# Optimization experiments

Hardware: AMD Instinct MI355X
Metric: run time of the kernel (lower is better)

Reference implementation:

```python
import jax, jax.numpy as jnp
import numpy as np

D = 512
H = 8
DV = D // H  # 64
NEG_INF = -1e30


def setup_inputs() -> dict:
    key = jax.random.key(0)
    ks = jax.random.split(key, 10)
    B, S = 4, 2048
    x = jax.random.normal(ks[0], (B, D, S), dtype=jnp.float32)
    mask = jnp.ones((B, S), dtype=jnp.float32)
    s = 1.0 / np.sqrt(D)
    sv = 1.0 / np.sqrt(D)
    # per-head Linear(d -> dv) weights stacked: [H, dv, d] (torch Linear layout W @ x)
    Wq = jax.random.uniform(ks[1], (H, DV, D), jnp.float32, -s, s)
    bq = jax.random.uniform(ks[2], (H, DV), jnp.float32, -s, s)
    Wk = jax.random.uniform(ks[3], (H, DV, D), jnp.float32, -s, s)
    bk = jax.random.uniform(ks[4], (H, DV), jnp.float32, -s, s)
    Wv = jax.random.uniform(ks[5], (H, DV, D), jnp.float32, -s, s)
    bv = jax.random.uniform(ks[6], (H, DV), jnp.float32, -s, s)
    W0 = jax.random.uniform(ks[7], (D, D), jnp.float32, -sv, sv)
    b0 = jax.random.uniform(ks[8], (D,), jnp.float32, -sv, sv)
    return {"x": x, "mask": mask, "Wq": Wq, "bq": bq, "Wk": Wk, "bk": bk,
            "Wv": Wv, "bv": bv, "W0": W0, "b0": b0}


def reference(x, mask, Wq, bq, Wk, bk, Wv, bv, W0, b0):
    # x: [B, d, S] -> xt: [B, S, d]
    xt = jnp.transpose(x, (0, 2, 1))
    # fused per-head projections: [B, H, S, dv]
    q = jnp.einsum('bsd,hed->bhse', xt, Wq) + bq[None, :, None, :]
    k = jnp.einsum('bsd,hed->bhse', xt, Wk) + bk[None, :, None, :]
    v = jnp.einsum('bsd,hed->bhse', xt, Wv) + bv[None, :, None, :]
    dv = q.shape[-1]
    scores = jnp.einsum('bhse,bhte->bhst', q, k) * (1.0 / np.sqrt(dv))
    # mask_logits (QANet style): keep where mask==1, else -1e30; mask over key dim
    h_mask = mask[:, None, None, :]  # [B,1,1,S]
    scores = scores * h_mask + (1.0 - h_mask) * NEG_INF
    p = jax.nn.softmax(scores, axis=-1)
    # zero out fully-masked query rows via v_mask on query dim
    p = p * mask[:, None, :, None]
    out = jnp.einsum('bhst,bhte->bhse', p, v)  # [B,H,S,dv]
    # concat heads along feature dim -> [B, S, d]
    B, _, S, _ = out.shape
    heads = jnp.transpose(out, (0, 2, 1, 3)).reshape(B, S, -1)
    y = heads @ W0.T + b0  # output projection
    return jnp.transpose(y, (0, 2, 1))  # [B, d, S]
```

## Files before the change

### kernel.cpp

```cpp
#include <hip/hip_runtime.h>

#define B_  4
#define D_  512
#define H_  8
#define DV_ 64
#define S_  2048

typedef __bf16 bf16;
typedef bf16  bf16x8 __attribute__((ext_vector_type(8)));
typedef bf16  bf16x4 __attribute__((ext_vector_type(4)));
typedef float f32x4  __attribute__((ext_vector_type(4)));

#define MFMA(a, b, c) __builtin_amdgcn_mfma_f32_16x16x32_bf16((a), (b), (c), 0, 0, 0)

#define GLOAD_LDS(g, l)                                                     \
    __builtin_amdgcn_global_load_lds(                                       \
        (const __attribute__((address_space(1))) void*)(g),                 \
        (__attribute__((address_space(3))) void*)(l), 16, 0, 0)

#define WAIT_VMCNT(n)                                                       \
    __builtin_amdgcn_s_waitcnt(((n) & 15) | (((n) >> 4) << 14) | (7 << 4) | (15 << 8))

__global__ __launch_bounds__(256) void prep(
    const float* __restrict__ x, const float* __restrict__ Wq,
    const float* __restrict__ Wk, const float* __restrict__ Wv,
    const float* __restrict__ W0, bf16* __restrict__ xb, bf16* __restrict__ Wb) {
    const int bid = blockIdx.x;
    if (bid < 4096) {
        __shared__ float tile[32][33];
        const int sblk = bid % 64;
        const int dblk = (bid / 64) % 16;
        const int b    = bid / 1024;
        const int d0 = dblk * 32, s0 = sblk * 32;
        const int tx = threadIdx.x & 31;
        const int ty = threadIdx.x >> 5;
        const float* xp = x + (size_t)b * D_ * S_;
#pragma unroll
        for (int i = 0; i < 32; i += 8)
            tile[ty + i][tx] = xp[(size_t)(d0 + ty + i) * S_ + s0 + tx];
        __syncthreads();
        bf16* xbp = xb + ((size_t)b * S_ + s0) * D_ + d0;
#pragma unroll
        for (int i = 0; i < 32; i += 8)
            xbp[(size_t)(ty + i) * D_ + tx] = (bf16)tile[tx][ty + i];
    } else {
        const int f0 = ((bid - 4096) * 256 + threadIdx.x) * 16;
        const int src = f0 >> 18;
        const int off = f0 & 262143;
        const float* W = (src == 0) ? Wq : (src == 1) ? Wk : (src == 2) ? Wv : W0;
        float4 v0 = *(const float4*)&W[off];
        float4 v1 = *(const float4*)&W[off + 4];
        float4 v2 = *(const float4*)&W[off + 8];
        float4 v3 = *(const float4*)&W[off + 12];
        bf16x8 h0 = {(bf16)v0.x, (bf16)v0.y, (bf16)v0.z, (bf16)v0.w,
                     (bf16)v1.x, (bf16)v1.y, (bf16)v1.z, (bf16)v1.w};
        bf16x8 h1 = {(bf16)v2.x, (bf16)v2.y, (bf16)v2.z, (bf16)v2.w,
                     (bf16)v3.x, (bf16)v3.y, (bf16)v3.z, (bf16)v3.w};
        *(bf16x8*)&Wb[f0]     = h0;
        *(bf16x8*)&Wb[f0 + 8] = h1;
    }
}

__global__ __launch_bounds__(256) void gemm_qkv(
    const bf16* __restrict__ A, const bf16* __restrict__ Wb,
    const float* __restrict__ bq, const float* __restrict__ bk,
    const float* __restrict__ bv,
    bf16* __restrict__ Q, bf16* __restrict__ K, bf16* __restrict__ Vt) {
    __shared__ union {
        struct { bf16 A[8192]; bf16 B[8192]; } s;
        bf16 T[128][132];
    } sm;

    const int tid = threadIdx.x;
    const int w = tid >> 6, lane = tid & 63;
    const int m16 = lane & 15, quad = lane >> 4;
    const int wr = w & 1, wc = w >> 1;

    const int nblk = blockIdx.x % 12;
    const int mblk = blockIdx.x / 12;
    const int m0 = mblk * 128, n0 = nblk * 128;

    f32x4 acc[4][4];
#pragma unroll
    for (int i = 0; i < 4; ++i)
#pragma unroll
        for (int j = 0; j < 4; ++j) acc[i][j] = (f32x4){0.f, 0.f, 0.f, 0.f};

    for (int k0 = 0; k0 < D_; k0 += 64) {
        __syncthreads();
#pragma unroll
        for (int i = 0; i < 4; ++i) {
            const int c  = w * 4 + i;
            const int mt = c >> 1, kk = c & 1;
            const int row = mt * 16 + m16;
            const int col = k0 + kk * 32 + quad * 8;
            GLOAD_LDS(&A[(size_t)(m0 + row) * D_ + col],  &sm.s.A[(c * 64 + lane) * 8]);
            GLOAD_LDS(&Wb[(size_t)(n0 + row) * D_ + col], &sm.s.B[(c * 64 + lane) * 8]);
        }
        __syncthreads();
#pragma unroll
        for (int kk = 0; kk < 2; ++kk) {
            bf16x8 af[4], bfv[4];
#pragma unroll
            for (int t = 0; t < 4; ++t) {
                af[t]  = *(const bf16x8*)&sm.s.A[(((wr * 4 + t) * 2 + kk) * 64 + lane) * 8];
                bfv[t] = *(const bf16x8*)&sm.s.B[(((wc * 4 + t) * 2 + kk) * 64 + lane) * 8];
            }
#pragma unroll
            for (int mt = 0; mt < 4; ++mt)
#pragma unroll
                for (int nt = 0; nt < 4; ++nt)
                    acc[mt][nt] = MFMA(af[mt], bfv[nt], acc[mt][nt]);
        }
    }

    const int proj = n0 >> 9;
    const float* bias = (proj == 0) ? bq : (proj == 1) ? bk : bv;

    if (proj == 2) {
#pragma unroll
        for (int mt = 0; mt < 4; ++mt)
#pragma unroll
            for (int nt = 0; nt < 4; ++nt) {
                const int nr = (n0 + wc * 64 + nt * 16 + m16) & 511;
                const int h = nr >> 6, e = nr & 63;
                const float bia = bias[nr];
                const int srow = m0 + wr * 64 + mt * 16 + quad * 4;
                const int b = srow >> 11, s = srow & 2047;
                const int s2 = (s & ~31) | (quad * 8 + (mt & 1) * 4);
                bf16x4 hv;
#pragma unroll
                for (int r = 0; r < 4; ++r) hv[r] = (bf16)(acc[mt][nt][r] + bia);
                *(bf16x4*)&Vt[(((size_t)b * H_ + h) * DV_ + e) * S_ + s2] = hv;
            }
    } else {
        __syncthreads();
#pragma unroll
        for (int mt = 0; mt < 4; ++mt)
#pragma unroll
            for (int nt = 0; nt < 4; ++nt) {
                const int nloc = wc * 64 + nt * 16 + m16;
                const float bia = bias[(n0 + nloc) & 511];
#pragma unroll
                for (int r = 0; r < 4; ++r)
                    sm.T[wr * 64 + mt * 16 + quad * 4 + r][nloc] =
                        (bf16)(acc[mt][nt][r] + bia);
            }
        __syncthreads();
        const int rloc = tid >> 1, cb = (tid & 1) * 64;
        const int M = m0 + rloc, b = M >> 11, s = M & 2047;
        const int nrb = (n0 + cb) & 511;
        const int h = nrb >> 6;
        bf16* dst = ((proj == 0) ? Q : K) + (((size_t)b * H_ + h) * S_ + s) * DV_;
#pragma unroll
        for (int u = 0; u < 8; ++u)
            *(bf16x8*)&dst[u * 8] = *(const bf16x8*)&sm.T[rloc][cb + u * 8];
    }
}

__global__ __launch_bounds__(256, 2) void flash_attn(
    const bf16* __restrict__ Q, const bf16* __restrict__ K, const bf16* __restrict__ Vt,
    const float* __restrict__ mask, bf16* __restrict__ heads) {
    __shared__ union {
        struct {
            bf16 Kl[2][4][2048];
            bf16 Vl[2][4][2048];
            float Ms[2048];
        } s;
        struct { float O[64][65]; float L[64]; } red;
    } sm;

    const int bidx = blockIdx.x;
    const int qblk = bidx & 31;
    const int h    = (bidx >> 5) & 7;
    const int b    = bidx >> 8;
    const int q0   = qblk * 64;

    const int tid = threadIdx.x;
    const int w = tid >> 6, lane = tid & 63;
    const int m16 = lane & 15, quad = lane >> 4;

    const bf16* Qp = Q  + ((size_t)b * H_ + h) * S_ * DV_;
    const bf16* Kp = K  + ((size_t)b * H_ + h) * S_ * DV_;
    const bf16* Vp = Vt + ((size_t)b * H_ + h) * DV_ * S_;
    const float* mp = mask + (size_t)b * S_;

    const int krow = lane >> 3;
    const int kcol = ((lane & 7) ^ krow) * 8;
    const int vrow = lane >> 2;
    const int vcol = ((lane & 3) ^ (vrow & 3)) * 8;

    bf16x8 qf[4][2];
#pragma unroll
    for (int qt = 0; qt < 4; ++qt)
#pragma unroll
        for (int kk = 0; kk < 2; ++kk) {
            bf16x8 v = *(const bf16x8*)&Qp[(size_t)(q0 + qt * 16 + m16) * DV_ +
                                           kk * 32 + quad * 8];
#pragma unroll
            for (int i = 0; i < 8; ++i) v[i] = (bf16)((float)v[i] * 0.125f);
            qf[qt][kk] = v;
        }

    bf16x8 ones;
#pragma unroll
    for (int i = 0; i < 8; ++i) ones[i] = (bf16)1.0f;

    f32x4 o[4][4];
    f32x4 lacc[4];
#pragma unroll
    for (int mt = 0; mt < 4; ++mt)
#pragma unroll
        for (int qt = 0; qt < 4; ++qt) o[mt][qt] = (f32x4){0.f, 0.f, 0.f, 0.f};
#pragma unroll
    for (int qt = 0; qt < 4; ++qt) lacc[qt] = (f32x4){0.f, 0.f, 0.f, 0.f};

#pragma unroll
    for (int p = 0; p < 2; ++p)
        GLOAD_LDS(&mp[(p * 256 + tid) * 4], &sm.s.Ms[(p * 256 + tid) * 4]);
    {
        const int tw = w * 32;
#pragma unroll
        for (int p = 0; p < 4; ++p)
            GLOAD_LDS(&Kp[(size_t)(tw + p * 8 + krow) * DV_ + kcol],
                      &sm.s.Kl[0][w][(p * 64 + lane) * 8]);
#pragma unroll
        for (int p = 0; p < 4; ++p)
            GLOAD_LDS(&Vp[(size_t)(p * 16 + vrow) * S_ + tw + vcol],
                      &sm.s.Vl[0][w][(p * 64 + lane) * 8]);
    }
    __syncthreads();

    for (int i = 0; i < 16; ++i) {
        const int tw = i * 128 + w * 32;
        if (i < 15) {
            const int twn = tw + 128;
            const int nb = (i + 1) & 1;
#pragma unroll
            for (int p = 0; p < 4; ++p)
                GLOAD_LDS(&Kp[(size_t)(twn + p * 8 + krow) * DV_ + kcol],
                          &sm.s.Kl[nb][w][(p * 64 + lane) * 8]);
#pragma unroll
            for (int p = 0; p < 4; ++p)
                GLOAD_LDS(&Vp[(size_t)(p * 16 + vrow) * S_ + twn + vcol],
                          &sm.s.Vl[nb][w][(p * 64 + lane) * 8]);
            WAIT_VMCNT(8);
        } else {
            WAIT_VMCNT(0);
        }
        const int buf = i & 1;

        bf16x8 kf[2][2];
#pragma unroll
        for (int tt = 0; tt < 2; ++tt)
#pragma unroll
            for (int kk = 0; kk < 2; ++kk)
                kf[tt][kk] = *(const bf16x8*)&sm.s.Kl[buf][w][
                    ((tt * 16 + m16) * 8 + ((kk * 4 + quad) ^ (m16 & 7))) * 8];
        bf16x8 vf[4];
#pragma unroll
        for (int mt = 0; mt < 4; ++mt)
            vf[mt] = *(const bf16x8*)&sm.s.Vl[buf][w][
                ((mt * 16 + m16) * 4 + (quad ^ (m16 & 3))) * 8];
        const f32x4 mq0 = *(const f32x4*)&sm.s.Ms[tw + quad * 4];
        const f32x4 mq1 = *(const f32x4*)&sm.s.Ms[tw + 16 + quad * 4];

        f32x4 sc[2][4];
#pragma unroll
        for (int tt = 0; tt < 2; ++tt)
#pragma unroll
            for (int qt = 0; qt < 4; ++qt) sc[tt][qt] = (f32x4){0.f, 0.f, 0.f, 0.f};
#pragma unroll
        for (int kk = 0; kk < 2; ++kk)
#pragma unroll
            for (int tt = 0; tt < 2; ++tt)
#pragma unroll
                for (int qt = 0; qt < 4; ++qt)
                    sc[tt][qt] = MFMA(kf[tt][kk], qf[qt][kk], sc[tt][qt]);

        f32x4 ng0, ng1;
#pragma unroll
        for (int r = 0; r < 4; ++r) {
            ng0[r] = (1.0f - mq0[r]) * -1e30f;
            ng1[r] = (1.0f - mq1[r]) * -1e30f;
        }
        bf16x8 pf[4];
#pragma unroll
        for (int qt = 0; qt < 4; ++qt)
#pragma unroll
            for (int r = 0; r < 4; ++r) {
                pf[qt][r]     = (bf16)__expf(sc[0][qt][r] * mq0[r] + ng0[r]);
                pf[qt][4 + r] = (bf16)__expf(sc[1][qt][r] * mq1[r] + ng1[r]);
            }

#pragma unroll
        for (int mt = 0; mt < 4; ++mt)
#pragma unroll
            for (int qt = 0; qt < 4; ++qt) o[mt][qt] = MFMA(vf[mt], pf[qt], o[mt][qt]);
#pragma unroll
        for (int qt = 0; qt < 4; ++qt) lacc[qt] = MFMA(ones, pf[qt], lacc[qt]);
    }

    __syncthreads();
#pragma unroll
    for (int ww = 0; ww < 4; ++ww) {
        if (w == ww) {
#pragma unroll
            for (int mt = 0; mt < 4; ++mt)
#pragma unroll
                for (int qt = 0; qt < 4; ++qt)
#pragma unroll
                    for (int r = 0; r < 4; ++r) {
                        float* slot = &sm.red.O[mt * 16 + quad * 4 + r][qt * 16 + m16];
                        *slot = (ww == 0) ? o[mt][qt][r] : (*slot + o[mt][qt][r]);
                    }
            if (quad == 0)
#pragma unroll
                for (int qt = 0; qt < 4; ++qt) {
                    float* ls = &sm.red.L[qt * 16 + m16];
                    *ls = (ww == 0) ? lacc[qt][0] : (*ls + lacc[qt][0]);
                }
        }
        __syncthreads();
    }

    const int ql = tid >> 2, ec = (tid & 3) * 16;
    const float l  = sm.red.L[ql];
    const float qm = mp[q0 + ql];
    const float inv = qm / l;
    bf16x8 hv[2];
#pragma unroll
    for (int c = 0; c < 2; ++c)
#pragma unroll
        for (int i = 0; i < 8; ++i)
            hv[c][i] = (bf16)(sm.red.O[ec + c * 8 + i][ql] * inv);
    bf16* dst = &heads[((size_t)b * S_ + q0 + ql) * D_ + h * DV_ + ec];
    *(bf16x8*)(dst)     = hv[0];
    *(bf16x8*)(dst + 8) = hv[1];
}

__global__ __launch_bounds__(256) void gemm_out(
    const bf16* __restrict__ A, const bf16* __restrict__ Wb,
    const float* __restrict__ b0, float* __restrict__ outp) {
    __shared__ bf16 Asl[8192];
    __shared__ bf16 Bsl[8192];

    const int tid = threadIdx.x;
    const int w = tid >> 6, lane = tid & 63;
    const int m16 = lane & 15, quad = lane >> 4;
    const int wr = w & 1, wc = w >> 1;

    const int nblk = blockIdx.x & 3;
    const int mblk = blockIdx.x >> 2;
    const int m0 = mblk * 128, n0 = nblk * 128;

    f32x4 acc[4][4];
#pragma unroll
    for (int i = 0; i < 4; ++i)
#pragma unroll
        for (int j = 0; j < 4; ++j) acc[i][j] = (f32x4){0.f, 0.f, 0.f, 0.f};

    for (int k0 = 0; k0 < D_; k0 += 64) {
        __syncthreads();
#pragma unroll
        for (int i = 0; i < 4; ++i) {
            const int c  = w * 4 + i;
            const int mt = c >> 1, kk = c & 1;
            const int row = mt * 16 + m16;
            const int col = k0 + kk * 32 + quad * 8;
            GLOAD_LDS(&A[(size_t)(m0 + row) * D_ + col], &Asl[(c * 64 + lane) * 8]);
            GLOAD_LDS(&Wb[(size_t)(1536 + n0 + row) * D_ + col], &Bsl[(c * 64 + lane) * 8]);
        }
        __syncthreads();
#pragma unroll
        for (int kk = 0; kk < 2; ++kk) {
            bf16x8 af[4], bfv[4];
#pragma unroll
            for (int t = 0; t < 4; ++t) {
                af[t]  = *(const bf16x8*)&Asl[(((wr * 4 + t) * 2 + kk) * 64 + lane) * 8];
                bfv[t] = *(const bf16x8*)&Bsl[(((wc * 4 + t) * 2 + kk) * 64 + lane) * 8];
            }
#pragma unroll
            for (int mt = 0; mt < 4; ++mt)
#pragma unroll
                for (int nt = 0; nt < 4; ++nt)
                    acc[mt][nt] = MFMA(af[mt], bfv[nt], acc[mt][nt]);
        }
    }

#pragma unroll
    for (int mt = 0; mt < 4; ++mt)
#pragma unroll
        for (int nt = 0; nt < 4; ++nt) {
            const int n = n0 + wc * 64 + nt * 16 + m16;
            const float bia = b0[n];
            const int srow = m0 + wr * 64 + mt * 16 + quad * 4;
            const int b = srow >> 11, s = srow & 2047;
            float4 vv;
            vv.x = acc[mt][nt][0] + bia;
            vv.y = acc[mt][nt][1] + bia;
            vv.z = acc[mt][nt][2] + bia;
            vv.w = acc[mt][nt][3] + bia;
            *(float4*)&outp[((size_t)b * D_ + n) * S_ + s] = vv;
        }
}

extern "C" void kernel_launch(void* const* d_in, const int* in_sizes, int n_in,
                              void* d_out, int out_size, void* d_ws, size_t ws_size,
                              hipStream_t stream) {
    const float* x    = (const float*)d_in[0];
    const float* mask = (const float*)d_in[1];
    const float* Wq   = (const float*)d_in[2];
    const float* bq   = (const float*)d_in[3];
    const float* Wk   = (const float*)d_in[4];
    const float* bk   = (const float*)d_in[5];
    const float* Wv   = (const float*)d_in[6];
    const float* bv   = (const float*)d_in[7];
    const float* W0   = (const float*)d_in[8];
    const float* b0   = (const float*)d_in[9];
    float* out = (float*)d_out;

    char* ws = (char*)d_ws;
    const size_t SEG = (size_t)B_ * S_ * D_ * sizeof(bf16);
    bf16* xb    = (bf16*)(ws);
    bf16* Qb    = (bf16*)(ws + SEG);
    bf16* Kb    = (bf16*)(ws + 2 * SEG);
    bf16* Vt    = (bf16*)(ws + 3 * SEG);
    bf16* Wb    = (bf16*)(ws + 4 * SEG);
    bf16* heads = xb;

    prep<<<dim3(4096 + 256), dim3(256), 0, stream>>>(x, Wq, Wk, Wv, W0, xb, Wb);
    gemm_qkv<<<dim3(64 * 12), dim3(256), 0, stream>>>(xb, Wb, bq, bk, bv, Qb, Kb, Vt);
    flash_attn<<<dim3(B_ * H_ * (S_ / 64)), dim3(256), 0, stream>>>(Qb, Kb, Vt, mask, heads);
    gemm_out<<<dim3(64 * 4), dim3(256), 0, stream>>>(heads, Wb, b0, out);
}
```

Baseline: 203.5 us.

## Halve GEMM M-tiles, drop LDS swizzles in attention, use exp2 softmax

```diff
diff --git a/kernel.cpp b/kernel.cpp
--- a/kernel.cpp
+++ b/kernel.cpp
@@ -5,6 +5,7 @@
 #define H_  8
 #define DV_ 64
 #define S_  2048
+#define LOG2E 1.4426950408889634f
 
 typedef __bf16 bf16;
 typedef bf16  bf16x8 __attribute__((ext_vector_type(8)));
@@ -67,47 +68,52 @@
     const float* __restrict__ bv,
     bf16* __restrict__ Q, bf16* __restrict__ K, bf16* __restrict__ Vt) {
     __shared__ union {
-        struct { bf16 A[8192]; bf16 B[8192]; } s;
-        bf16 T[128][132];
+        struct { bf16 A[4096]; bf16 B[8192]; } s;
+        bf16 T[64][132];
     } sm;
 
     const int tid = threadIdx.x;
     const int w = tid >> 6, lane = tid & 63;
     const int m16 = lane & 15, quad = lane >> 4;
+    const int lr = lane & 15, lc = lane >> 4;
     const int wr = w & 1, wc = w >> 1;
 
     const int nblk = blockIdx.x % 12;
     const int mblk = blockIdx.x / 12;
-    const int m0 = mblk * 128, n0 = nblk * 128;
-
-    f32x4 acc[4][4];
-#pragma unroll
-    for (int i = 0; i < 4; ++i)
+    const int m0 = mblk * 64, n0 = nblk * 128;
+
+    f32x4 acc[2][4];
+#pragma unroll
+    for (int i = 0; i < 2; ++i)
 #pragma unroll
         for (int j = 0; j < 4; ++j) acc[i][j] = (f32x4){0.f, 0.f, 0.f, 0.f};
 
     for (int k0 = 0; k0 < D_; k0 += 64) {
         __syncthreads();
 #pragma unroll
-        for (int i = 0; i < 4; ++i) {
-            const int c  = w * 4 + i;
-            const int mt = c >> 1, kk = c & 1;
-            const int row = mt * 16 + m16;
-            const int col = k0 + kk * 32 + quad * 8;
-            GLOAD_LDS(&A[(size_t)(m0 + row) * D_ + col],  &sm.s.A[(c * 64 + lane) * 8]);
-            GLOAD_LDS(&Wb[(size_t)(n0 + row) * D_ + col], &sm.s.B[(c * 64 + lane) * 8]);
+        for (int j = 0; j < 2; ++j) {
+            const int c = 2 * w + j;
+            GLOAD_LDS(&A[(size_t)(m0 + (c >> 1) * 16 + lr) * D_ + k0 + (c & 1) * 32 + lc * 8],
+                      &sm.s.A[(c * 64 + lane) * 8]);
+        }
+#pragma unroll
+        for (int j = 0; j < 4; ++j) {
+            const int c = 4 * w + j;
+            GLOAD_LDS(&Wb[(size_t)(n0 + (c >> 1) * 16 + lr) * D_ + k0 + (c & 1) * 32 + lc * 8],
+                      &sm.s.B[(c * 64 + lane) * 8]);
         }
         __syncthreads();
 #pragma unroll
         for (int kk = 0; kk < 2; ++kk) {
-            bf16x8 af[4], bfv[4];
-#pragma unroll
-            for (int t = 0; t < 4; ++t) {
-                af[t]  = *(const bf16x8*)&sm.s.A[(((wr * 4 + t) * 2 + kk) * 64 + lane) * 8];
-                bfv[t] = *(const bf16x8*)&sm.s.B[(((wc * 4 + t) * 2 + kk) * 64 + lane) * 8];
-            }
-#pragma unroll
-            for (int mt = 0; mt < 4; ++mt)
+            bf16x8 af[2], bfv[4];
+#pragma unroll
+            for (int mt = 0; mt < 2; ++mt)
+                af[mt] = *(const bf16x8*)&sm.s.A[(((wr * 2 + mt) * 2 + kk) * 64 + lane) * 8];
+#pragma unroll
+            for (int nt = 0; nt < 4; ++nt)
+                bfv[nt] = *(const bf16x8*)&sm.s.B[(((wc * 4 + nt) * 2 + kk) * 64 + lane) * 8];
+#pragma unroll
+            for (int mt = 0; mt < 2; ++mt)
 #pragma unroll
                 for (int nt = 0; nt < 4; ++nt)
                     acc[mt][nt] = MFMA(af[mt], bfv[nt], acc[mt][nt]);
@@ -119,15 +125,15 @@
 
     if (proj == 2) {
 #pragma unroll
-        for (int mt = 0; mt < 4; ++mt)
+        for (int mt = 0; mt < 2; ++mt)
 #pragma unroll
             for (int nt = 0; nt < 4; ++nt) {
                 const int nr = (n0 + wc * 64 + nt * 16 + m16) & 511;
                 const int h = nr >> 6, e = nr & 63;
                 const float bia = bias[nr];
-                const int srow = m0 + wr * 64 + mt * 16 + quad * 4;
+                const int srow = m0 + wr * 32 + mt * 16 + quad * 4;
                 const int b = srow >> 11, s = srow & 2047;
-                const int s2 = (s & ~31) | (quad * 8 + (mt & 1) * 4);
+                const int s2 = (s & ~31) | (quad * 8 + mt * 4);
                 bf16x4 hv;
 #pragma unroll
                 for (int r = 0; r < 4; ++r) hv[r] = (bf16)(acc[mt][nt][r] + bia);
@@ -136,24 +142,24 @@
     } else {
         __syncthreads();
 #pragma unroll
-        for (int mt = 0; mt < 4; ++mt)
+        for (int mt = 0; mt < 2; ++mt)
 #pragma unroll
             for (int nt = 0; nt < 4; ++nt) {
                 const int nloc = wc * 64 + nt * 16 + m16;
                 const float bia = bias[(n0 + nloc) & 511];
 #pragma unroll
                 for (int r = 0; r < 4; ++r)
-                    sm.T[wr * 64 + mt * 16 + quad * 4 + r][nloc] =
+                    sm.T[wr * 32 + mt * 16 + quad * 4 + r][nloc] =
                         (bf16)(acc[mt][nt][r] + bia);
             }
         __syncthreads();
-        const int rloc = tid >> 1, cb = (tid & 1) * 64;
+        const int rloc = tid >> 2, cb = (tid & 3) * 32;
         const int M = m0 + rloc, b = M >> 11, s = M & 2047;
-        const int nrb = (n0 + cb) & 511;
-        const int h = nrb >> 6;
-        bf16* dst = ((proj == 0) ? Q : K) + (((size_t)b * H_ + h) * S_ + s) * DV_;
-#pragma unroll
-        for (int u = 0; u < 8; ++u)
+        const int ncol = (n0 + cb) & 511;
+        const int h = ncol >> 6, e0 = ncol & 63;
+        bf16* dst = ((proj == 0) ? Q : K) + (((size_t)b * H_ + h) * S_ + s) * DV_ + e0;
+#pragma unroll
+        for (int u = 0; u < 4; ++u)
             *(bf16x8*)&dst[u * 8] = *(const bf16x8*)&sm.T[rloc][cb + u * 8];
     }
 }
@@ -165,10 +171,10 @@
         struct {
             bf16 Kl[2][4][2048];
             bf16 Vl[2][4][2048];
-            float Ms[2048];
         } s;
         struct { float O[64][65]; float L[64]; } red;
     } sm;
+    __shared__ float Ms[2048];
 
     const int bidx = blockIdx.x;
     const int qblk = bidx & 31;
@@ -179,16 +185,18 @@
     const int tid = threadIdx.x;
     const int w = tid >> 6, lane = tid & 63;
     const int m16 = lane & 15, quad = lane >> 4;
+    const int lr = lane & 15, lc = lane >> 4;
 
     const bf16* Qp = Q  + ((size_t)b * H_ + h) * S_ * DV_;
     const bf16* Kp = K  + ((size_t)b * H_ + h) * S_ * DV_;
     const bf16* Vp = Vt + ((size_t)b * H_ + h) * DV_ * S_;
     const float* mp = mask + (size_t)b * S_;
 
-    const int krow = lane >> 3;
-    const int kcol = ((lane & 7) ^ krow) * 8;
-    const int vrow = lane >> 2;
-    const int vcol = ((lane & 3) ^ (vrow & 3)) * 8;
+    const bf16* kgp = Kp + (size_t)(w * 32 + lr) * DV_ + lc * 8;
+    const bf16* vgp0 = Vp + (size_t)(lr) * S_      + w * 32 + lc * 8;
+    const bf16* vgp1 = Vp + (size_t)(16 + lr) * S_ + w * 32 + lc * 8;
+    const bf16* vgp2 = Vp + (size_t)(32 + lr) * S_ + w * 32 + lc * 8;
+    const bf16* vgp3 = Vp + (size_t)(48 + lr) * S_ + w * 32 + lc * 8;
 
     bf16x8 qf[4][2];
 #pragma unroll
@@ -215,55 +223,58 @@
 #pragma unroll
     for (int qt = 0; qt < 4; ++qt) lacc[qt] = (f32x4){0.f, 0.f, 0.f, 0.f};
 
-#pragma unroll
-    for (int p = 0; p < 2; ++p)
-        GLOAD_LDS(&mp[(p * 256 + tid) * 4], &sm.s.Ms[(p * 256 + tid) * 4]);
     {
-        const int tw = w * 32;
-#pragma unroll
-        for (int p = 0; p < 4; ++p)
-            GLOAD_LDS(&Kp[(size_t)(tw + p * 8 + krow) * DV_ + kcol],
-                      &sm.s.Kl[0][w][(p * 64 + lane) * 8]);
-#pragma unroll
-        for (int p = 0; p < 4; ++p)
-            GLOAD_LDS(&Vp[(size_t)(p * 16 + vrow) * S_ + tw + vcol],
-                      &sm.s.Vl[0][w][(p * 64 + lane) * 8]);
-    }
+        const int mi = tid * 8;
+        const float4 a = *(const float4*)&mp[mi];
+        const float4 c = *(const float4*)&mp[mi + 4];
+        Ms[mi + 0] = a.x * LOG2E; Ms[mi + 1] = a.y * LOG2E;
+        Ms[mi + 2] = a.z * LOG2E; Ms[mi + 3] = a.w * LOG2E;
+        Ms[mi + 4] = c.x * LOG2E; Ms[mi + 5] = c.y * LOG2E;
+        Ms[mi + 6] = c.z * LOG2E; Ms[mi + 7] = c.w * LOG2E;
+    }
+#pragma unroll
+    for (int c = 0; c < 4; ++c) {
+        GLOAD_LDS(kgp + (c >> 1) * 16 * DV_ + (c & 1) * 32, &sm.s.Kl[0][w][(c * 64 + lane) * 8]);
+    }
+    GLOAD_LDS(vgp0, &sm.s.Vl[0][w][(0 * 64 + lane) * 8]);
+    GLOAD_LDS(vgp1, &sm.s.Vl[0][w][(1 * 64 + lane) * 8]);
+    GLOAD_LDS(vgp2, &sm.s.Vl[0][w][(2 * 64 + lane) * 8]);
+    GLOAD_LDS(vgp3, &sm.s.Vl[0][w][(3 * 64 + lane) * 8]);
     __syncthreads();
 
     for (int i = 0; i < 16; ++i) {
         const int tw = i * 128 + w * 32;
+        const int buf = i & 1;
+
         if (i < 15) {
-            const int twn = tw + 128;
-            const int nb = (i + 1) & 1;
-#pragma unroll
-            for (int p = 0; p < 4; ++p)
-                GLOAD_LDS(&Kp[(size_t)(twn + p * 8 + krow) * DV_ + kcol],
-                          &sm.s.Kl[nb][w][(p * 64 + lane) * 8]);
-#pragma unroll
-            for (int p = 0; p < 4; ++p)
-                GLOAD_LDS(&Vp[(size_t)(p * 16 + vrow) * S_ + twn + vcol],
-                          &sm.s.Vl[nb][w][(p * 64 + lane) * 8]);
+            kgp  += 128 * DV_;
+            vgp0 += 128; vgp1 += 128; vgp2 += 128; vgp3 += 128;
+            const int nb = buf ^ 1;
+#pragma unroll
+            for (int c = 0; c < 4; ++c)
+                GLOAD_LDS(kgp + (c >> 1) * 16 * DV_ + (c & 1) * 32,
+                          &sm.s.Kl[nb][w][(c * 64 + lane) * 8]);
+            GLOAD_LDS(vgp0, &sm.s.Vl[nb][w][(0 * 64 + lane) * 8]);
+            GLOAD_LDS(vgp1, &sm.s.Vl[nb][w][(1 * 64 + lane) * 8]);
+            GLOAD_LDS(vgp2, &sm.s.Vl[nb][w][(2 * 64 + lane) * 8]);
+            GLOAD_LDS(vgp3, &sm.s.Vl[nb][w][(3 * 64 + lane) * 8]);
             WAIT_VMCNT(8);
         } else {
             WAIT_VMCNT(0);
         }
-        const int buf = i & 1;
 
         bf16x8 kf[2][2];
 #pragma unroll
         for (int tt = 0; tt < 2; ++tt)
 #pragma unroll
             for (int kk = 0; kk < 2; ++kk)
-                kf[tt][kk] = *(const bf16x8*)&sm.s.Kl[buf][w][
-                    ((tt * 16 + m16) * 8 + ((kk * 4 + quad) ^ (m16 & 7))) * 8];
+                kf[tt][kk] = *(const bf16x8*)&sm.s.Kl[buf][w][((tt * 2 + kk) * 64 + lane) * 8];
         bf16x8 vf[4];
 #pragma unroll
         for (int mt = 0; mt < 4; ++mt)
-            vf[mt] = *(const bf16x8*)&sm.s.Vl[buf][w][
-                ((mt * 16 + m16) * 4 + (quad ^ (m16 & 3))) * 8];
-        const f32x4 mq0 = *(const f32x4*)&sm.s.Ms[tw + quad * 4];
-        const f32x4 mq1 = *(const f32x4*)&sm.s.Ms[tw + 16 + quad * 4];
+            vf[mt] = *(const bf16x8*)&sm.s.Vl[buf][w][(mt * 64 + lane) * 8];
+        const f32x4 mq0 = *(const f32x4*)&Ms[tw + quad * 4];
+        const f32x4 mq1 = *(const f32x4*)&Ms[tw + 16 + quad * 4];
 
         f32x4 sc[2][4];
 #pragma unroll
@@ -281,16 +292,16 @@
         f32x4 ng0, ng1;
 #pragma unroll
         for (int r = 0; r < 4; ++r) {
-            ng0[r] = (1.0f - mq0[r]) * -1e30f;
-            ng1[r] = (1.0f - mq1[r]) * -1e30f;
+            ng0[r] = (LOG2E - mq0[r]) * -7e29f;
+            ng1[r] = (LOG2E - mq1[r]) * -7e29f;
         }
         bf16x8 pf[4];
 #pragma unroll
         for (int qt = 0; qt < 4; ++qt)
 #pragma unroll
             for (int r = 0; r < 4; ++r) {
-                pf[qt][r]     = (bf16)__expf(sc[0][qt][r] * mq0[r] + ng0[r]);
-                pf[qt][4 + r] = (bf16)__expf(sc[1][qt][r] * mq1[r] + ng1[r]);
+                pf[qt][r]     = (bf16)exp2f(sc[0][qt][r] * mq0[r] + ng0[r]);
+                pf[qt][4 + r] = (bf16)exp2f(sc[1][qt][r] * mq1[r] + ng1[r]);
             }
 
 #pragma unroll
@@ -342,46 +353,51 @@
 __global__ __launch_bounds__(256) void gemm_out(
     const bf16* __restrict__ A, const bf16* __restrict__ Wb,
     const float* __restrict__ b0, float* __restrict__ outp) {
-    __shared__ bf16 Asl[8192];
+    __shared__ bf16 Asl[4096];
     __shared__ bf16 Bsl[8192];
 
     const int tid = threadIdx.x;
     const int w = tid >> 6, lane = tid & 63;
     const int m16 = lane & 15, quad = lane >> 4;
+    const int lr = lane & 15, lc = lane >> 4;
     const int wr = w & 1, wc = w >> 1;
 
     const int nblk = blockIdx.x & 3;
     const int mblk = blockIdx.x >> 2;
-    const int m0 = mblk * 128, n0 = nblk * 128;
-
-    f32x4 acc[4][4];
-#pragma unroll
-    for (int i = 0; i < 4; ++i)
+    const int m0 = mblk * 64, n0 = nblk * 128;
+
+    f32x4 acc[2][4];
+#pragma unroll
+    for (int i = 0; i < 2; ++i)
 #pragma unroll
         for (int j = 0; j < 4; ++j) acc[i][j] = (f32x4){0.f, 0.f, 0.f, 0.f};
 
     for (int k0 = 0; k0 < D_; k0 += 64) {
         __syncthreads();
 #pragma unroll
-        for (int i = 0; i < 4; ++i) {
-            const int c  = w * 4 + i;
-            const int mt = c >> 1, kk = c & 1;
-            const int row = mt * 16 + m16;
-            const int col = k0 + kk * 32 + quad * 8;
-            GLOAD_LDS(&A[(size_t)(m0 + row) * D_ + col], &Asl[(c * 64 + lane) * 8]);
-            GLOAD_LDS(&Wb[(size_t)(1536 + n0 + row) * D_ + col], &Bsl[(c * 64 + lane) * 8]);
+        for (int j = 0; j < 2; ++j) {
+            const int c = 2 * w + j;
+            GLOAD_LDS(&A[(size_t)(m0 + (c >> 1) * 16 + lr) * D_ + k0 + (c & 1) * 32 + lc * 8],
+                      &Asl[(c * 64 + lane) * 8]);
+        }
+#pragma unroll
+        for (int j = 0; j < 4; ++j) {
+            const int c = 4 * w + j;
+            GLOAD_LDS(&Wb[(size_t)(1536 + n0 + (c >> 1) * 16 + lr) * D_ + k0 + (c & 1) * 32 + lc * 8],
+                      &Bsl[(c * 64 + lane) * 8]);
         }
         __syncthreads();
 #pragma unroll
         for (int kk = 0; kk < 2; ++kk) {
-            bf16x8 af[4], bfv[4];
-#pragma unroll
-            for (int t = 0; t < 4; ++t) {
-                af[t]  = *(const bf16x8*)&Asl[(((wr * 4 + t) * 2 + kk) * 64 + lane) * 8];
-                bfv[t] = *(const bf16x8*)&Bsl[(((wc * 4 + t) * 2 + kk) * 64 + lane) * 8];
-            }
-#pragma unroll
-            for (int mt = 0; mt < 4; ++mt)
+            bf16x8 af[2], bfv[4];
+#pragma unroll
+            for (int mt = 0; mt < 2; ++mt)
+                af[mt] = *(const bf16x8*)&Asl[(((wr * 2 + mt) * 2 + kk) * 64 + lane) * 8];
+#pragma unroll
+            for (int nt = 0; nt < 4; ++nt)
+                bfv[nt] = *(const bf16x8*)&Bsl[(((wc * 4 + nt) * 2 + kk) * 64 + lane) * 8];
+#pragma unroll
+            for (int mt = 0; mt < 2; ++mt)
 #pragma unroll
                 for (int nt = 0; nt < 4; ++nt)
                     acc[mt][nt] = MFMA(af[mt], bfv[nt], acc[mt][nt]);
@@ -389,12 +405,12 @@
     }
 
 #pragma unroll
-    for (int mt = 0; mt < 4; ++mt)
+    for (int mt = 0; mt < 2; ++mt)
 #pragma unroll
         for (int nt = 0; nt < 4; ++nt) {
             const int n = n0 + wc * 64 + nt * 16 + m16;
             const float bia = b0[n];
-            const int srow = m0 + wr * 64 + mt * 16 + quad * 4;
+            const int srow = m0 + wr * 32 + mt * 16 + quad * 4;
             const int b = srow >> 11, s = srow & 2047;
             float4 vv;
             vv.x = acc[mt][nt][0] + bia;
@@ -430,7 +446,7 @@
     bf16* heads = xb;
 
     prep<<<dim3(4096 + 256), dim3(256), 0, stream>>>(x, Wq, Wk, Wv, W0, xb, Wb);
-    gemm_qkv<<<dim3(64 * 12), dim3(256), 0, stream>>>(xb, Wb, bq, bk, bv, Qb, Kb, Vt);
+    gemm_qkv<<<dim3(128 * 12), dim3(256), 0, stream>>>(xb, Wb, bq, bk, bv, Qb, Kb, Vt);
     flash_attn<<<dim3(B_ * H_ * (S_ / 64)), dim3(256), 0, stream>>>(Qb, Kb, Vt, mask, heads);
-    gemm_out<<<dim3(64 * 4), dim3(256), 0, stream>>>(heads, Wb, b0, out);
+    gemm_out<<<dim3(128 * 4), dim3(256), 0, stream>>>(heads, Wb, b0, out);
 }
```

Result: slower. 227.4 us (+11.7%).
